# Performance work log

Hardware: AMD Instinct MI355X
Metric: run time of the kernel (lower is better)

Reference implementation:

```python
import jax, jax.numpy as jnp
import numpy as np

NUM_NODES = 100000
NUM_EDGES = 1600000
DIM = 64
TAU = 0.5
EPS = 1e-12
SURGERY_EPS = 1e-6


def setup_inputs() -> dict:
    key = jax.random.key(0)
    k1, k2, k3, k4, k5 = jax.random.split(key, 5)
    x = jax.random.normal(k1, (NUM_NODES, DIM), dtype=jnp.float32)
    edge_index = jax.random.randint(k2, (2, NUM_EDGES), 0, NUM_NODES, dtype=jnp.int64)
    edge_weight = jax.random.uniform(k3, (NUM_EDGES,), dtype=jnp.float32)
    # nn.Linear weights (no bias): y = x @ W.T
    W_self = jax.random.normal(k4, (DIM, DIM), dtype=jnp.float32) / np.sqrt(DIM)
    W_neigh = jax.random.normal(k5, (DIM, DIM), dtype=jnp.float32) / np.sqrt(DIM)
    return {"x": x, "edge_index": edge_index, "edge_weight": edge_weight,
            "W_self": W_self, "W_neigh": W_neigh}


def reference(x, edge_index, edge_weight, W_self, W_neigh):
    num_nodes = x.shape[0]
    row, col = edge_index[0], edge_index[1]

    # --- Ollivier-Ricci (LLY limit-free combinatorial lower-bound) curvature per edge ---
    deg = jax.ops.segment_sum(edge_weight, row, num_segments=num_nodes)  # weighted out-degree
    inv_du = 1.0 / jnp.maximum(deg[row], EPS)
    inv_dv = 1.0 / jnp.maximum(deg[col], EPS)
    kappa = 2.0 * inv_du + 2.0 * inv_dv - 2.0  # [E]

    # --- CFL-stable step size for the Ricci flow ---
    delta_t = 0.5 / (jnp.max(jnp.abs(kappa)) + 1e-6)

    # --- Ricci-flow half step: dw/dt = -kappa * w ---
    w_half = jnp.maximum(edge_weight * (1.0 - 0.5 * delta_t * kappa), 0.0)

    # --- metric surgery: drop degenerate edges (implemented as a zero-weight mask,
    #     keeping edge count static so the kernel is jit-compatible) ---
    mask = w_half > SURGERY_EPS
    w_half = jnp.where(mask, w_half, 0.0)

    # --- row normalisation ---
    row_sum = jax.ops.segment_sum(w_half, row, num_segments=num_nodes)
    w_norm = w_half / jnp.maximum(row_sum[row], EPS)

    # --- Laplacian off-diagonals: L_uv = -w_norm  =>  -L_uv = w_norm ---
    minus_L = w_norm

    # --- incident mean curvature per node (over surviving edges) -> curvature gate ---
    cnt = jax.ops.segment_sum(mask.astype(x.dtype), row, num_segments=num_nodes)
    k_sum = jax.ops.segment_sum(jnp.where(mask, kappa, 0.0), row, num_segments=num_nodes)
    mean_kappa = k_sum / jnp.maximum(cnt, 1.0)
    rho = jax.nn.sigmoid(mean_kappa)  # [N]

    # --- gated message passing ---
    h_self = x @ W_self.T    # [N, D]
    h_neigh = x @ W_neigh.T  # [N, D]
    msg = minus_L[:, None] * h_neigh[col]                      # [E, D] gather + scale
    neigh_aggr = jax.ops.segment_sum(msg, row, num_segments=num_nodes)  # scatter-add

    # h0 buffer == first-forward x (detached)
    out = rho[:, None] * h_self + neigh_aggr + TAU * x
    return out, edge_index, w_norm
```

## Files before the change

kernel.cpp:

```cpp
#include <hip/hip_runtime.h>
#include <math.h>

#define NNODES 100000
#define NEDGES 1600000
#define DIM 64
#define TAU 0.5f
#define EPSF 1e-12f
#define SEPS 1e-6f

#define K 256
#define RPB 391
#define TILE 4096
#define EPT 16
#define CAP 7168
#define MAXK_GRID 512

typedef unsigned long long ull;
typedef unsigned short u16;
typedef __attribute__((ext_vector_type(8))) short bf16x8;
typedef __attribute__((ext_vector_type(4))) float f32x4;

__device__ __forceinline__ float bf2f(u16 h) {
    return __uint_as_float((unsigned)h << 16);
}
__device__ __forceinline__ u16 f2bf(float f) {
    unsigned u = __float_as_uint(f);
    u += 0x7FFFu + ((u >> 16) & 1);
    return (u16)(u >> 16);
}

__global__ __launch_bounds__(256) void k_init(int* __restrict__ bcur) {
    bcur[threadIdx.x] = threadIdx.x * CAP;
}

__global__ __launch_bounds__(256) void k_bin(const int* __restrict__ ei, const float* __restrict__ w,
                                             int* __restrict__ bcur, ull* __restrict__ arena,
                                             int E, int N) {
    __shared__ ull stg[TILE];
    __shared__ unsigned char bkt[TILE];
    __shared__ int cnt[K], lscan[K], gbase[K], cur[K], sc[K];
    __shared__ int tot;
    int t = threadIdx.x;
    int e0 = blockIdx.x * TILE;
    cnt[t] = 0; cur[t] = 0;
    __syncthreads();
    ull rec[EPT];
    int bb[EPT];
#pragma unroll
    for (int j = 0; j < EPT; j++) {
        int e = e0 + t + j * 256;
        bb[j] = -1;
        if (e < E) {
            int r = min(max(ei[e], 0), N - 1);
            int c = min(max(ei[E + e], 0), N - 1);
            float wv = w[e];
            int b = r / RPB, lr = r - b * RPB;
            rec[j] = ((ull)__float_as_uint(wv) << 32) | (unsigned)(c | (lr << 17));
            bb[j] = b;
            atomicAdd(&cnt[b], 1);
        }
    }
    __syncthreads();
    int v = cnt[t];
    sc[t] = v;
    __syncthreads();
    for (int o = 1; o < K; o <<= 1) {
        int a = (t >= o) ? sc[t - o] : 0;
        __syncthreads();
        sc[t] += a;
        __syncthreads();
    }
    lscan[t] = sc[t] - v;
    if (v > 0) gbase[t] = atomicAdd(&bcur[t], v);
    if (t == K - 1) tot = sc[t];
    __syncthreads();
#pragma unroll
    for (int j = 0; j < EPT; j++) {
        if (bb[j] >= 0) {
            int p = lscan[bb[j]] + atomicAdd(&cur[bb[j]], 1);
            stg[p] = rec[j];
            bkt[p] = (unsigned char)bb[j];
        }
    }
    __syncthreads();
    int T = tot;
    for (int i = t; i < T; i += 256) {
        int b = bkt[i];
        size_t pos = (size_t)gbase[b] + (i - lscan[b]);
        if (pos < (size_t)(b + 1) * CAP) arena[pos] = stg[i];
    }
}

__global__ __launch_bounds__(256) void k_sort(const int* __restrict__ bcur,
                                              ull* __restrict__ arena,
                                              float* __restrict__ invdeg,
                                              int* __restrict__ off, int* __restrict__ degi,
                                              int N) {
    __shared__ ull stg[CAP];
    __shared__ int hist[RPB];
    __shared__ float degl[RPB];
    __shared__ int cur[RPB];
    __shared__ int sc[512];
    int t = threadIdx.x, b = blockIdx.x;
    int base = b * CAP;
    int cnt = min(bcur[b] - base, CAP);
    for (int i = t; i < RPB; i += 256) { hist[i] = 0; degl[i] = 0.0f; cur[i] = 0; }
    __syncthreads();
    for (int i = t; i < cnt; i += 256) {
        ull rec = arena[base + i];
        stg[i] = rec;
        int lr = (int)((rec >> 17) & 0x1FF);
        atomicAdd(&hist[lr], 1);
        atomicAdd(&degl[lr], __uint_as_float((unsigned)(rec >> 32)));
    }
    __syncthreads();
    int v0 = (t < RPB) ? hist[t] : 0;
    int v1 = (t + 256 < RPB) ? hist[t + 256] : 0;
    sc[t] = v0; sc[t + 256] = v1;
    __syncthreads();
    for (int o = 1; o < 512; o <<= 1) {
        int a = (t >= o) ? sc[t - o] : 0;
        int c2 = (t + 256 >= o) ? sc[t + 256 - o] : 0;
        __syncthreads();
        sc[t] += a; sc[t + 256] += c2;
        __syncthreads();
    }
    int ex0 = sc[t] - v0, ex1 = sc[t + 256] - v1;
    hist[t] = ex0;
    if (t + 256 < RPB) hist[t + 256] = ex1;
    int rn0 = b * RPB + t;
    if (rn0 < N) {
        off[rn0] = base + ex0; degi[rn0] = v0;
        invdeg[rn0] = 1.0f / fmaxf(degl[t], EPSF);
    }
    int rn1 = rn0 + 256;
    if (t + 256 < RPB && rn1 < N) {
        off[rn1] = base + ex1; degi[rn1] = v1;
        invdeg[rn1] = 1.0f / fmaxf(degl[t + 256], EPSF);
    }
    __syncthreads();
    int2* out2 = (int2*)arena;
    for (int i = t; i < cnt; i += 256) {
        ull rec = stg[i];
        int lr = (int)((rec >> 17) & 0x1FF);
        int p = hist[lr] + atomicAdd(&cur[lr], 1);
        out2[base + p] = make_int2((int)(rec & 0x1FFFF), (int)(unsigned)(rec >> 32));
    }
}

__global__ __launch_bounds__(256) void k_maxk(const int* __restrict__ ei,
                                              const float* __restrict__ invdeg,
                                              float* __restrict__ maxabs, int E, int N) {
    float m = 0.0f;
    int stride = gridDim.x * 256;
    for (int e = blockIdx.x * 256 + threadIdx.x; e < E; e += stride) {
        int r = min(max(ei[e], 0), N - 1);
        int c = min(max(ei[E + e], 0), N - 1);
        m = fmaxf(m, fabsf(2.0f * invdeg[r] + 2.0f * invdeg[c] - 2.0f));
    }
    for (int o = 32; o > 0; o >>= 1) m = fmaxf(m, __shfl_down(m, o, 64));
    __shared__ float red[4];
    int lane = threadIdx.x & 63, wid = threadIdx.x >> 6;
    if (lane == 0) red[wid] = m;
    __syncthreads();
    if (threadIdx.x == 0) {
        float bm = fmaxf(fmaxf(red[0], red[1]), fmaxf(red[2], red[3]));
        atomicMax((unsigned int*)maxabs, __float_as_uint(bm));
    }
}

__global__ void k_node(const int* __restrict__ off, const int* __restrict__ degi,
                       const float* __restrict__ invdeg,
                       const int2* __restrict__ csr, const float* __restrict__ maxabs,
                       float* __restrict__ rho, float* __restrict__ row_sum, int N) {
    int n = blockIdx.x * blockDim.x + threadIdx.x;
    if (n >= N) return;
    int s = off[n], e2 = s + degi[n];
    float dt = 0.5f / (*maxabs + 1e-6f);
    float a = 2.0f * invdeg[n] - 2.0f;
    float rs = 0.0f, ct = 0.0f, ks = 0.0f;
    for (int i = s; i < e2; i++) {
        int2 pr = csr[i];
        float we = __int_as_float(pr.y);
        float kap = a + 2.0f * invdeg[pr.x];
        float wh = fmaxf(we * (1.0f - 0.5f * dt * kap), 0.0f);
        if (wh > SEPS) { rs += wh; ct += 1.0f; ks += kap; }
    }
    float mk = ks / fmaxf(ct, 1.0f);
    rho[n] = 1.0f / (1.0f + expf(-mk));
    row_sum[n] = rs;
}

#define WL(mp, d, kk) (((mp) * 64 + (d)) * 72 + (kk))
__global__ __launch_bounds__(256) void k_gemm(const float* __restrict__ x,
                                              const float* __restrict__ Wself,
                                              const float* __restrict__ Wneigh,
                                              const float* __restrict__ rho,
                                              u16* __restrict__ hneigh_h,
                                              float* __restrict__ out, int N) {
    __shared__ u16 wlds[4 * 64 * 72];
    int t = threadIdx.x;
    for (int i = t; i < 4096; i += 256) {
        int d = i >> 6, k = i & 63;
        float v = Wself[i];
        u16 h = f2bf(v);
        u16 lo = f2bf(v - bf2f(h));
        wlds[WL(0, d, k)] = h;
        wlds[WL(1, d, k)] = lo;
        v = Wneigh[i];
        h = f2bf(v);
        lo = f2bf(v - bf2f(h));
        wlds[WL(2, d, k)] = h;
        wlds[WL(3, d, k)] = lo;
    }
    __syncthreads();
    int w = t >> 6, l = t & 63;
    int m = l & 15, kg = l >> 4;
    int n0 = blockIdx.x * 64 + w * 16;
    if (n0 >= N) return;
    int nodeA = n0 + m;
    bf16x8 ah[2], al[2];
#pragma unroll
    for (int ks = 0; ks < 2; ks++) {
        float v[8];
        if (nodeA < N) {
            const float4* xp = (const float4*)(x + (size_t)nodeA * 64 + ks * 32 + kg * 8);
            float4 v0 = xp[0], v1 = xp[1];
            v[0] = v0.x; v[1] = v0.y; v[2] = v0.z; v[3] = v0.w;
            v[4] = v1.x; v[5] = v1.y; v[6] = v1.z; v[7] = v1.w;
        } else {
#pragma unroll
            for (int j = 0; j < 8; j++) v[j] = 0.0f;
        }
#pragma unroll
        for (int j = 0; j < 8; j++) {
            u16 h = f2bf(v[j]);
            u16 lo = f2bf(v[j] - bf2f(h));
            ah[ks][j] = (short)h;
            al[ks][j] = (short)lo;
        }
    }
    f32x4 accS[4], accN[4];
#pragma unroll
    for (int dt = 0; dt < 4; dt++) {
        accS[dt] = (f32x4){0.0f, 0.0f, 0.0f, 0.0f};
        accN[dt] = (f32x4){0.0f, 0.0f, 0.0f, 0.0f};
    }
#pragma unroll
    for (int dt = 0; dt < 4; dt++) {
        int d = dt * 16 + m;
#pragma unroll
        for (int ks = 0; ks < 2; ks++) {
            int kof = ks * 32 + kg * 8;
            bf16x8 bsh = *(const bf16x8*)&wlds[WL(0, d, kof)];
            bf16x8 bsl = *(const bf16x8*)&wlds[WL(1, d, kof)];
            bf16x8 bnh = *(const bf16x8*)&wlds[WL(2, d, kof)];
            bf16x8 bnl = *(const bf16x8*)&wlds[WL(3, d, kof)];
            accS[dt] = __builtin_amdgcn_mfma_f32_16x16x32_bf16(ah[ks], bsh, accS[dt], 0, 0, 0);
            accS[dt] = __builtin_amdgcn_mfma_f32_16x16x32_bf16(al[ks], bsh, accS[dt], 0, 0, 0);
            accS[dt] = __builtin_amdgcn_mfma_f32_16x16x32_bf16(ah[ks], bsl, accS[dt], 0, 0, 0);
            accN[dt] = __builtin_amdgcn_mfma_f32_16x16x32_bf16(ah[ks], bnh, accN[dt], 0, 0, 0);
            accN[dt] = __builtin_amdgcn_mfma_f32_16x16x32_bf16(al[ks], bnh, accN[dt], 0, 0, 0);
            accN[dt] = __builtin_amdgcn_mfma_f32_16x16x32_bf16(ah[ks], bnl, accN[dt], 0, 0, 0);
        }
    }
    int rbase = kg * 4;
#pragma unroll
    for (int r = 0; r < 4; r++) {
        int nn = n0 + rbase + r;
        if (nn >= N) continue;
        float rh = rho[nn];
#pragma unroll
        for (int dt = 0; dt < 4; dt++) {
            int d = dt * 16 + m;
            size_t idx = (size_t)nn * 64 + d;
            out[idx] = rh * accS[dt][r] + TAU * x[idx];
            hneigh_h[idx] = f2bf(accN[dt][r]);
        }
    }
}

__global__ __launch_bounds__(256) void k_aggr(const int* __restrict__ off,
                                              const int* __restrict__ degi,
                                              const float* __restrict__ invdeg,
                                              const int2* __restrict__ csr,
                                              const float* __restrict__ row_sum,
                                              const float* __restrict__ maxabs,
                                              const u16* __restrict__ hneigh_h,
                                              float* __restrict__ out, int N) {
    int t = threadIdx.x;
    int lane = t & 63;
    int q = lane & 15;
    int g = lane >> 4;
    int n = blockIdx.x * 4 + (t >> 6);
    if (n >= N) return;
    int s = off[n], end = s + degi[n];
    float dt = 0.5f / (*maxabs + 1e-6f);
    float c1 = -0.5f * dt;
    float a = 2.0f * invdeg[n] - 2.0f;
    float inv_rs = 1.0f / fmaxf(row_sum[n], EPSF);
    const ushort4* hn4 = (const ushort4*)hneigh_h;
    float a0 = 0.0f, a1 = 0.0f, a2 = 0.0f, a3 = 0.0f;
    int i = s;
    for (; i + 16 <= end; i += 16) {
        int2 p0 = csr[i + g];
        int2 p1 = csr[i + 4 + g];
        int2 p2 = csr[i + 8 + g];
        int2 p3 = csr[i + 12 + g];
        ushort4 h0 = hn4[(unsigned)((p0.x << 4) | q)];
        ushort4 h1 = hn4[(unsigned)((p1.x << 4) | q)];
        ushort4 h2 = hn4[(unsigned)((p2.x << 4) | q)];
        ushort4 h3 = hn4[(unsigned)((p3.x << 4) | q)];
        float k0 = fmaf(2.0f, invdeg[p0.x], a), k1 = fmaf(2.0f, invdeg[p1.x], a);
        float k2 = fmaf(2.0f, invdeg[p2.x], a), k3 = fmaf(2.0f, invdeg[p3.x], a);
        float w0 = __int_as_float(p0.y) * fmaf(c1, k0, 1.0f);
        float w1 = __int_as_float(p1.y) * fmaf(c1, k1, 1.0f);
        float w2 = __int_as_float(p2.y) * fmaf(c1, k2, 1.0f);
        float w3 = __int_as_float(p3.y) * fmaf(c1, k3, 1.0f);
        w0 = (w0 > SEPS) ? w0 : 0.0f;
        w1 = (w1 > SEPS) ? w1 : 0.0f;
        w2 = (w2 > SEPS) ? w2 : 0.0f;
        w3 = (w3 > SEPS) ? w3 : 0.0f;
        a0 = fmaf(w0, bf2f(h0.x), a0); a1 = fmaf(w0, bf2f(h0.y), a1);
        a2 = fmaf(w0, bf2f(h0.z), a2); a3 = fmaf(w0, bf2f(h0.w), a3);
        a0 = fmaf(w1, bf2f(h1.x), a0); a1 = fmaf(w1, bf2f(h1.y), a1);
        a2 = fmaf(w1, bf2f(h1.z), a2); a3 = fmaf(w1, bf2f(h1.w), a3);
        a0 = fmaf(w2, bf2f(h2.x), a0); a1 = fmaf(w2, bf2f(h2.y), a1);
        a2 = fmaf(w2, bf2f(h2.z), a2); a3 = fmaf(w2, bf2f(h2.w), a3);
        a0 = fmaf(w3, bf2f(h3.x), a0); a1 = fmaf(w3, bf2f(h3.y), a1);
        a2 = fmaf(w3, bf2f(h3.z), a2); a3 = fmaf(w3, bf2f(h3.w), a3);
    }
    for (; i + 8 <= end; i += 8) {
        int2 p0 = csr[i + g];
        int2 p1 = csr[i + 4 + g];
        ushort4 h0 = hn4[(unsigned)((p0.x << 4) | q)];
        ushort4 h1 = hn4[(unsigned)((p1.x << 4) | q)];
        float k0 = fmaf(2.0f, invdeg[p0.x], a), k1 = fmaf(2.0f, invdeg[p1.x], a);
        float w0 = __int_as_float(p0.y) * fmaf(c1, k0, 1.0f);
        float w1 = __int_as_float(p1.y) * fmaf(c1, k1, 1.0f);
        w0 = (w0 > SEPS) ? w0 : 0.0f;
        w1 = (w1 > SEPS) ? w1 : 0.0f;
        a0 = fmaf(w0, bf2f(h0.x), a0); a1 = fmaf(w0, bf2f(h0.y), a1);
        a2 = fmaf(w0, bf2f(h0.z), a2); a3 = fmaf(w0, bf2f(h0.w), a3);
        a0 = fmaf(w1, bf2f(h1.x), a0); a1 = fmaf(w1, bf2f(h1.y), a1);
        a2 = fmaf(w1, bf2f(h1.z), a2); a3 = fmaf(w1, bf2f(h1.w), a3);
    }
    for (; i < end; i += 4) {
        int e = i + g;
        bool v = e < end;
        int2 p = make_int2(0, 0);
        if (v) p = csr[e];
        ushort4 h = hn4[(unsigned)((p.x << 4) | q)];
        float kk = fmaf(2.0f, invdeg[p.x], a);
        float wv = __int_as_float(p.y) * fmaf(c1, kk, 1.0f);
        wv = (v && wv > SEPS) ? wv : 0.0f;
        a0 = fmaf(wv, bf2f(h.x), a0);
        a1 = fmaf(wv, bf2f(h.y), a1);
        a2 = fmaf(wv, bf2f(h.z), a2);
        a3 = fmaf(wv, bf2f(h.w), a3);
    }
    a0 += __shfl_xor(a0, 16, 64);
    a1 += __shfl_xor(a1, 16, 64);
    a2 += __shfl_xor(a2, 16, 64);
    a3 += __shfl_xor(a3, 16, 64);
    a0 += __shfl_xor(a0, 32, 64);
    a1 += __shfl_xor(a1, 32, 64);
    a2 += __shfl_xor(a2, 32, 64);
    a3 += __shfl_xor(a3, 32, 64);
    if (g == 0) {
        float4* o4 = (float4*)(out + (size_t)n * 64);
        float4 o = o4[q];
        o.x += a0 * inv_rs;
        o.y += a1 * inv_rs;
        o.z += a2 * inv_rs;
        o.w += a3 * inv_rs;
        o4[q] = o;
    }
}

__global__ void k_final(const int* __restrict__ ei, const float* __restrict__ w,
                        const float* __restrict__ invdeg, const float* __restrict__ row_sum,
                        const float* __restrict__ maxabs,
                        float* __restrict__ out_ei, float* __restrict__ out_wn, int E, int N) {
    int e = blockIdx.x * blockDim.x + threadIdx.x;
    if (e >= E) return;
    int r0 = ei[e], c0 = ei[E + e];
    int r = min(max(r0, 0), N - 1);
    int c = min(max(c0, 0), N - 1);
    float dt = 0.5f / (*maxabs + 1e-6f);
    float kap = 2.0f * invdeg[r] + 2.0f * invdeg[c] - 2.0f;
    float wh = fmaxf(w[e] * (1.0f - 0.5f * dt * kap), 0.0f);
    if (wh <= SEPS) wh = 0.0f;
    out_wn[e] = wh / fmaxf(row_sum[r], EPSF);
    out_ei[e] = (float)r0;
    out_ei[E + e] = (float)c0;
}

extern "C" void kernel_launch(void* const* d_in, const int* in_sizes, int n_in,
                              void* d_out, int out_size, void* d_ws, size_t ws_size,
                              hipStream_t stream) {
    (void)in_sizes; (void)n_in; (void)out_size; (void)ws_size;
    const int N = NNODES, E = NEDGES;

    const float* x      = (const float*)d_in[0];
    const int*   ei     = (const int*)d_in[1];
    const float* w      = (const float*)d_in[2];
    const float* Wself  = (const float*)d_in[3];
    const float* Wneigh = (const float*)d_in[4];

    float* out    = (float*)d_out;
    float* out_ei = out + (size_t)N * DIM;
    float* out_wn = out_ei + 2 * (size_t)E;

    ull*  arena = (ull*)out_ei;
    int2* csr   = (int2*)out_ei;

    float* invdeg  = (float*)d_ws;
    int*   off     = (int*)d_ws + (size_t)N;
    int*   degi    = (int*)d_ws + 2 * (size_t)N;
    float* rho     = (float*)d_ws + 3 * (size_t)N;
    float* row_sum = rho + (size_t)N;
    float* maxabs  = row_sum + (size_t)N;
    int*   bcur    = (int*)(maxabs + 4);
    u16*   hneigh_h = (u16*)((float*)d_ws + 5 * (size_t)N + 288);

    hipMemsetAsync((void*)maxabs, 0, 4 * sizeof(float), stream);

    k_init<<<1, 256, 0, stream>>>(bcur);
    k_bin<<<(E + TILE - 1) / TILE, 256, 0, stream>>>(ei, w, bcur, arena, E, N);
    k_sort<<<K, 256, 0, stream>>>(bcur, arena, invdeg, off, degi, N);
    k_maxk<<<MAXK_GRID, 256, 0, stream>>>(ei, invdeg, maxabs, E, N);
    k_node<<<(N + 255) / 256, 256, 0, stream>>>(off, degi, invdeg, csr, maxabs, rho, row_sum, N);
    k_gemm<<<(N + 63) / 64, 256, 0, stream>>>(x, Wself, Wneigh, rho, hneigh_h, out, N);
    k_aggr<<<(N + 3) / 4, 256, 0, stream>>>(off, degi, invdeg, csr, row_sum, maxabs,
                                            hneigh_h, out, N);
    k_final<<<(E + 255) / 256, 256, 0, stream>>>(ei, w, invdeg, row_sum, maxabs,
                                                 out_ei, out_wn, E, N);
}
```

Baseline: 261.8 us.

## Precompute half-step weights into CSR and replace per-node loop with bin-parallel kernel

The per-node curvature/row-sum kernel, which had one thread walk each node's edges serially, is replaced by a bin-level kernel. It processes each sorted bucket's edges in parallel, using shared-memory atomics per local row. That kernel also writes the surgery-masked half-step weight back into the CSR record and keeps the local row index in the upper bits of the column field. The aggregation kernel then reads the precomputed weight directly and no longer gathers invdeg per edge or recomputes kappa. The costs are an extra write pass over the CSR array and a mask on every column index.

```diff
diff --git a/kernel.cpp b/kernel.cpp
--- a/kernel.cpp
+++ b/kernel.cpp
@@ -144,7 +144,7 @@
         ull rec = stg[i];
         int lr = (int)((rec >> 17) & 0x1FF);
         int p = hist[lr] + atomicAdd(&cur[lr], 1);
-        out2[base + p] = make_int2((int)(rec & 0x1FFFF), (int)(unsigned)(rec >> 32));
+        out2[base + p] = make_int2((int)(rec & 0x3FFFFFF), (int)(unsigned)(rec >> 32));
     }
 }
 
@@ -169,26 +169,49 @@
     }
 }
 
-__global__ void k_node(const int* __restrict__ off, const int* __restrict__ degi,
-                       const float* __restrict__ invdeg,
-                       const int2* __restrict__ csr, const float* __restrict__ maxabs,
-                       float* __restrict__ rho, float* __restrict__ row_sum, int N) {
-    int n = blockIdx.x * blockDim.x + threadIdx.x;
-    if (n >= N) return;
-    int s = off[n], e2 = s + degi[n];
+__global__ __launch_bounds__(256) void k_wh(const int* __restrict__ bcur,
+                                            const float* __restrict__ invdeg,
+                                            int2* __restrict__ csr,
+                                            const float* __restrict__ maxabs,
+                                            float* __restrict__ rho,
+                                            float* __restrict__ row_sum, int N) {
+    __shared__ float ivl[RPB], rs[RPB], ks[RPB];
+    __shared__ int ct[RPB];
+    int t = threadIdx.x, b = blockIdx.x;
+    int base = b * CAP;
+    int cnt = min(bcur[b] - base, CAP);
+    int r0 = b * RPB;
+    for (int i = t; i < RPB; i += 256) {
+        int rn = r0 + i;
+        ivl[i] = (rn < N) ? invdeg[rn] : 0.0f;
+        rs[i] = 0.0f; ks[i] = 0.0f; ct[i] = 0;
+    }
+    __syncthreads();
     float dt = 0.5f / (*maxabs + 1e-6f);
-    float a = 2.0f * invdeg[n] - 2.0f;
-    float rs = 0.0f, ct = 0.0f, ks = 0.0f;
-    for (int i = s; i < e2; i++) {
-        int2 pr = csr[i];
-        float we = __int_as_float(pr.y);
-        float kap = a + 2.0f * invdeg[pr.x];
-        float wh = fmaxf(we * (1.0f - 0.5f * dt * kap), 0.0f);
-        if (wh > SEPS) { rs += wh; ct += 1.0f; ks += kap; }
-    }
-    float mk = ks / fmaxf(ct, 1.0f);
-    rho[n] = 1.0f / (1.0f + expf(-mk));
-    row_sum[n] = rs;
+    for (int i = t; i < cnt; i += 256) {
+        int2 rec = csr[base + i];
+        int col = rec.x & 0x1FFFF;
+        int lr = rec.x >> 17;
+        float kap = 2.0f * (ivl[lr] + invdeg[col]) - 2.0f;
+        float wh = fmaxf(__int_as_float(rec.y) * (1.0f - 0.5f * dt * kap), 0.0f);
+        if (wh > SEPS) {
+            atomicAdd(&rs[lr], wh);
+            atomicAdd(&ks[lr], kap);
+            atomicAdd(&ct[lr], 1);
+        } else {
+            wh = 0.0f;
+        }
+        csr[base + i] = make_int2(rec.x, __float_as_int(wh));
+    }
+    __syncthreads();
+    for (int i = t; i < RPB; i += 256) {
+        int rn = r0 + i;
+        if (rn < N) {
+            float mk = ks[i] / fmaxf((float)ct[i], 1.0f);
+            rho[rn] = 1.0f / (1.0f + expf(-mk));
+            row_sum[rn] = rs[i];
+        }
+    }
 }
 
 #define WL(mp, d, kk) (((mp) * 64 + (d)) * 72 + (kk))
@@ -282,10 +305,8 @@
 
 __global__ __launch_bounds__(256) void k_aggr(const int* __restrict__ off,
                                               const int* __restrict__ degi,
-                                              const float* __restrict__ invdeg,
                                               const int2* __restrict__ csr,
                                               const float* __restrict__ row_sum,
-                                              const float* __restrict__ maxabs,
                                               const u16* __restrict__ hneigh_h,
                                               float* __restrict__ out, int N) {
     int t = threadIdx.x;
@@ -295,9 +316,6 @@
     int n = blockIdx.x * 4 + (t >> 6);
     if (n >= N) return;
     int s = off[n], end = s + degi[n];
-    float dt = 0.5f / (*maxabs + 1e-6f);
-    float c1 = -0.5f * dt;
-    float a = 2.0f * invdeg[n] - 2.0f;
     float inv_rs = 1.0f / fmaxf(row_sum[n], EPSF);
     const ushort4* hn4 = (const ushort4*)hneigh_h;
     float a0 = 0.0f, a1 = 0.0f, a2 = 0.0f, a3 = 0.0f;
@@ -307,20 +325,12 @@
         int2 p1 = csr[i + 4 + g];
         int2 p2 = csr[i + 8 + g];
         int2 p3 = csr[i + 12 + g];
-        ushort4 h0 = hn4[(unsigned)((p0.x << 4) | q)];
-        ushort4 h1 = hn4[(unsigned)((p1.x << 4) | q)];
-        ushort4 h2 = hn4[(unsigned)((p2.x << 4) | q)];
-        ushort4 h3 = hn4[(unsigned)((p3.x << 4) | q)];
-        float k0 = fmaf(2.0f, invdeg[p0.x], a), k1 = fmaf(2.0f, invdeg[p1.x], a);
-        float k2 = fmaf(2.0f, invdeg[p2.x], a), k3 = fmaf(2.0f, invdeg[p3.x], a);
-        float w0 = __int_as_float(p0.y) * fmaf(c1, k0, 1.0f);
-        float w1 = __int_as_float(p1.y) * fmaf(c1, k1, 1.0f);
-        float w2 = __int_as_float(p2.y) * fmaf(c1, k2, 1.0f);
-        float w3 = __int_as_float(p3.y) * fmaf(c1, k3, 1.0f);
-        w0 = (w0 > SEPS) ? w0 : 0.0f;
-        w1 = (w1 > SEPS) ? w1 : 0.0f;
-        w2 = (w2 > SEPS) ? w2 : 0.0f;
-        w3 = (w3 > SEPS) ? w3 : 0.0f;
+        ushort4 h0 = hn4[(unsigned)(((p0.x & 0x1FFFF) << 4) | q)];
+        ushort4 h1 = hn4[(unsigned)(((p1.x & 0x1FFFF) << 4) | q)];
+        ushort4 h2 = hn4[(unsigned)(((p2.x & 0x1FFFF) << 4) | q)];
+        ushort4 h3 = hn4[(unsigned)(((p3.x & 0x1FFFF) << 4) | q)];
+        float w0 = __int_as_float(p0.y), w1 = __int_as_float(p1.y);
+        float w2 = __int_as_float(p2.y), w3 = __int_as_float(p3.y);
         a0 = fmaf(w0, bf2f(h0.x), a0); a1 = fmaf(w0, bf2f(h0.y), a1);
         a2 = fmaf(w0, bf2f(h0.z), a2); a3 = fmaf(w0, bf2f(h0.w), a3);
         a0 = fmaf(w1, bf2f(h1.x), a0); a1 = fmaf(w1, bf2f(h1.y), a1);
@@ -333,13 +343,9 @@
     for (; i + 8 <= end; i += 8) {
         int2 p0 = csr[i + g];
         int2 p1 = csr[i + 4 + g];
-        ushort4 h0 = hn4[(unsigned)((p0.x << 4) | q)];
-        ushort4 h1 = hn4[(unsigned)((p1.x << 4) | q)];
-        float k0 = fmaf(2.0f, invdeg[p0.x], a), k1 = fmaf(2.0f, invdeg[p1.x], a);
-        float w0 = __int_as_float(p0.y) * fmaf(c1, k0, 1.0f);
-        float w1 = __int_as_float(p1.y) * fmaf(c1, k1, 1.0f);
-        w0 = (w0 > SEPS) ? w0 : 0.0f;
-        w1 = (w1 > SEPS) ? w1 : 0.0f;
+        ushort4 h0 = hn4[(unsigned)(((p0.x & 0x1FFFF) << 4) | q)];
+        ushort4 h1 = hn4[(unsigned)(((p1.x & 0x1FFFF) << 4) | q)];
+        float w0 = __int_as_float(p0.y), w1 = __int_as_float(p1.y);
         a0 = fmaf(w0, bf2f(h0.x), a0); a1 = fmaf(w0, bf2f(h0.y), a1);
         a2 = fmaf(w0, bf2f(h0.z), a2); a3 = fmaf(w0, bf2f(h0.w), a3);
         a0 = fmaf(w1, bf2f(h1.x), a0); a1 = fmaf(w1, bf2f(h1.y), a1);
@@ -350,10 +356,8 @@
         bool v = e < end;
         int2 p = make_int2(0, 0);
         if (v) p = csr[e];
-        ushort4 h = hn4[(unsigned)((p.x << 4) | q)];
-        float kk = fmaf(2.0f, invdeg[p.x], a);
-        float wv = __int_as_float(p.y) * fmaf(c1, kk, 1.0f);
-        wv = (v && wv > SEPS) ? wv : 0.0f;
+        ushort4 h = hn4[(unsigned)(((p.x & 0x1FFFF) << 4) | q)];
+        float wv = v ? __int_as_float(p.y) : 0.0f;
         a0 = fmaf(wv, bf2f(h.x), a0);
         a1 = fmaf(wv, bf2f(h.y), a1);
         a2 = fmaf(wv, bf2f(h.z), a2);
@@ -430,10 +434,9 @@
     k_bin<<<(E + TILE - 1) / TILE, 256, 0, stream>>>(ei, w, bcur, arena, E, N);
     k_sort<<<K, 256, 0, stream>>>(bcur, arena, invdeg, off, degi, N);
     k_maxk<<<MAXK_GRID, 256, 0, stream>>>(ei, invdeg, maxabs, E, N);
-    k_node<<<(N + 255) / 256, 256, 0, stream>>>(off, degi, invdeg, csr, maxabs, rho, row_sum, N);
+    k_wh<<<K, 256, 0, stream>>>(bcur, invdeg, csr, maxabs, rho, row_sum, N);
     k_gemm<<<(N + 63) / 64, 256, 0, stream>>>(x, Wself, Wneigh, rho, hneigh_h, out, N);
-    k_aggr<<<(N + 3) / 4, 256, 0, stream>>>(off, degi, invdeg, csr, row_sum, maxabs,
-                                            hneigh_h, out, N);
+    k_aggr<<<(N + 3) / 4, 256, 0, stream>>>(off, degi, csr, row_sum, hneigh_h, out, N);
     k_final<<<(E + 255) / 256, 256, 0, stream>>>(ei, w, invdeg, row_sum, maxabs,
                                                  out_ei, out_wn, E, N);
 }
```

New measurement: 269.3 us. +2.9%, slower.

## Fuse per-node curvature stats into aggregation kernel and drop k_node

Applied to the files above, without the earlier changes.

Removes the separate k_node pass over the CSR. k_aggr now accumulates row_sum, the curvature sum and the surviving-edge count during its neighbour loop. It then computes rho and applies the rho*h_self + tau*x epilogue, and k_gemm writes raw h_self. The memset is folded into k_init, and the 8-edge remainder loop is dropped. This removes one kernel launch and a full CSR and invdeg re-read, at the cost of a few extra reductions per aggregation and an x read moved into k_aggr.

```diff
diff --git a/kernel.cpp b/kernel.cpp
--- a/kernel.cpp
+++ b/kernel.cpp
@@ -29,8 +29,10 @@
     return (u16)(u >> 16);
 }
 
-__global__ __launch_bounds__(256) void k_init(int* __restrict__ bcur) {
+__global__ __launch_bounds__(256) void k_init(int* __restrict__ bcur,
+                                              float* __restrict__ maxabs) {
     bcur[threadIdx.x] = threadIdx.x * CAP;
+    if (threadIdx.x < 4) maxabs[threadIdx.x] = 0.0f;
 }
 
 __global__ __launch_bounds__(256) void k_bin(const int* __restrict__ ei, const float* __restrict__ w,
@@ -169,33 +171,10 @@
     }
 }
 
-__global__ void k_node(const int* __restrict__ off, const int* __restrict__ degi,
-                       const float* __restrict__ invdeg,
-                       const int2* __restrict__ csr, const float* __restrict__ maxabs,
-                       float* __restrict__ rho, float* __restrict__ row_sum, int N) {
-    int n = blockIdx.x * blockDim.x + threadIdx.x;
-    if (n >= N) return;
-    int s = off[n], e2 = s + degi[n];
-    float dt = 0.5f / (*maxabs + 1e-6f);
-    float a = 2.0f * invdeg[n] - 2.0f;
-    float rs = 0.0f, ct = 0.0f, ks = 0.0f;
-    for (int i = s; i < e2; i++) {
-        int2 pr = csr[i];
-        float we = __int_as_float(pr.y);
-        float kap = a + 2.0f * invdeg[pr.x];
-        float wh = fmaxf(we * (1.0f - 0.5f * dt * kap), 0.0f);
-        if (wh > SEPS) { rs += wh; ct += 1.0f; ks += kap; }
-    }
-    float mk = ks / fmaxf(ct, 1.0f);
-    rho[n] = 1.0f / (1.0f + expf(-mk));
-    row_sum[n] = rs;
-}
-
 #define WL(mp, d, kk) (((mp) * 64 + (d)) * 72 + (kk))
 __global__ __launch_bounds__(256) void k_gemm(const float* __restrict__ x,
                                               const float* __restrict__ Wself,
                                               const float* __restrict__ Wneigh,
-                                              const float* __restrict__ rho,
                                               u16* __restrict__ hneigh_h,
                                               float* __restrict__ out, int N) {
     __shared__ u16 wlds[4 * 64 * 72];
@@ -269,12 +248,11 @@
     for (int r = 0; r < 4; r++) {
         int nn = n0 + rbase + r;
         if (nn >= N) continue;
-        float rh = rho[nn];
 #pragma unroll
         for (int dt = 0; dt < 4; dt++) {
             int d = dt * 16 + m;
             size_t idx = (size_t)nn * 64 + d;
-            out[idx] = rh * accS[dt][r] + TAU * x[idx];
+            out[idx] = accS[dt][r];
             hneigh_h[idx] = f2bf(accN[dt][r]);
         }
     }
@@ -284,9 +262,10 @@
                                               const int* __restrict__ degi,
                                               const float* __restrict__ invdeg,
                                               const int2* __restrict__ csr,
-                                              const float* __restrict__ row_sum,
                                               const float* __restrict__ maxabs,
+                                              const float* __restrict__ x,
                                               const u16* __restrict__ hneigh_h,
+                                              float* __restrict__ row_sum,
                                               float* __restrict__ out, int N) {
     int t = threadIdx.x;
     int lane = t & 63;
@@ -298,9 +277,9 @@
     float dt = 0.5f / (*maxabs + 1e-6f);
     float c1 = -0.5f * dt;
     float a = 2.0f * invdeg[n] - 2.0f;
-    float inv_rs = 1.0f / fmaxf(row_sum[n], EPSF);
     const ushort4* hn4 = (const ushort4*)hneigh_h;
     float a0 = 0.0f, a1 = 0.0f, a2 = 0.0f, a3 = 0.0f;
+    float rs = 0.0f, ks = 0.0f, ct = 0.0f;
     int i = s;
     for (; i + 16 <= end; i += 16) {
         int2 p0 = csr[i + g];
@@ -317,10 +296,14 @@
         float w1 = __int_as_float(p1.y) * fmaf(c1, k1, 1.0f);
         float w2 = __int_as_float(p2.y) * fmaf(c1, k2, 1.0f);
         float w3 = __int_as_float(p3.y) * fmaf(c1, k3, 1.0f);
-        w0 = (w0 > SEPS) ? w0 : 0.0f;
-        w1 = (w1 > SEPS) ? w1 : 0.0f;
-        w2 = (w2 > SEPS) ? w2 : 0.0f;
-        w3 = (w3 > SEPS) ? w3 : 0.0f;
+        bool m0 = w0 > SEPS, m1 = w1 > SEPS, m2 = w2 > SEPS, m3 = w3 > SEPS;
+        w0 = m0 ? w0 : 0.0f;
+        w1 = m1 ? w1 : 0.0f;
+        w2 = m2 ? w2 : 0.0f;
+        w3 = m3 ? w3 : 0.0f;
+        rs += (w0 + w1) + (w2 + w3);
+        ks += ((m0 ? k0 : 0.0f) + (m1 ? k1 : 0.0f)) + ((m2 ? k2 : 0.0f) + (m3 ? k3 : 0.0f));
+        ct += ((m0 ? 1.0f : 0.0f) + (m1 ? 1.0f : 0.0f)) + ((m2 ? 1.0f : 0.0f) + (m3 ? 1.0f : 0.0f));
         a0 = fmaf(w0, bf2f(h0.x), a0); a1 = fmaf(w0, bf2f(h0.y), a1);
         a2 = fmaf(w0, bf2f(h0.z), a2); a3 = fmaf(w0, bf2f(h0.w), a3);
         a0 = fmaf(w1, bf2f(h1.x), a0); a1 = fmaf(w1, bf2f(h1.y), a1);
@@ -330,21 +313,6 @@
         a0 = fmaf(w3, bf2f(h3.x), a0); a1 = fmaf(w3, bf2f(h3.y), a1);
         a2 = fmaf(w3, bf2f(h3.z), a2); a3 = fmaf(w3, bf2f(h3.w), a3);
     }
-    for (; i + 8 <= end; i += 8) {
-        int2 p0 = csr[i + g];
-        int2 p1 = csr[i + 4 + g];
-        ushort4 h0 = hn4[(unsigned)((p0.x << 4) | q)];
-        ushort4 h1 = hn4[(unsigned)((p1.x << 4) | q)];
-        float k0 = fmaf(2.0f, invdeg[p0.x], a), k1 = fmaf(2.0f, invdeg[p1.x], a);
-        float w0 = __int_as_float(p0.y) * fmaf(c1, k0, 1.0f);
-        float w1 = __int_as_float(p1.y) * fmaf(c1, k1, 1.0f);
-        w0 = (w0 > SEPS) ? w0 : 0.0f;
-        w1 = (w1 > SEPS) ? w1 : 0.0f;
-        a0 = fmaf(w0, bf2f(h0.x), a0); a1 = fmaf(w0, bf2f(h0.y), a1);
-        a2 = fmaf(w0, bf2f(h0.z), a2); a3 = fmaf(w0, bf2f(h0.w), a3);
-        a0 = fmaf(w1, bf2f(h1.x), a0); a1 = fmaf(w1, bf2f(h1.y), a1);
-        a2 = fmaf(w1, bf2f(h1.z), a2); a3 = fmaf(w1, bf2f(h1.w), a3);
-    }
     for (; i < end; i += 4) {
         int e = i + g;
         bool v = e < end;
@@ -353,7 +321,11 @@
         ushort4 h = hn4[(unsigned)((p.x << 4) | q)];
         float kk = fmaf(2.0f, invdeg[p.x], a);
         float wv = __int_as_float(p.y) * fmaf(c1, kk, 1.0f);
-        wv = (v && wv > SEPS) ? wv : 0.0f;
+        bool m = v && (wv > SEPS);
+        wv = m ? wv : 0.0f;
+        rs += wv;
+        ks += m ? kk : 0.0f;
+        ct += m ? 1.0f : 0.0f;
         a0 = fmaf(wv, bf2f(h.x), a0);
         a1 = fmaf(wv, bf2f(h.y), a1);
         a2 = fmaf(wv, bf2f(h.z), a2);
@@ -363,18 +335,30 @@
     a1 += __shfl_xor(a1, 16, 64);
     a2 += __shfl_xor(a2, 16, 64);
     a3 += __shfl_xor(a3, 16, 64);
+    rs += __shfl_xor(rs, 16, 64);
+    ks += __shfl_xor(ks, 16, 64);
+    ct += __shfl_xor(ct, 16, 64);
     a0 += __shfl_xor(a0, 32, 64);
     a1 += __shfl_xor(a1, 32, 64);
     a2 += __shfl_xor(a2, 32, 64);
     a3 += __shfl_xor(a3, 32, 64);
+    rs += __shfl_xor(rs, 32, 64);
+    ks += __shfl_xor(ks, 32, 64);
+    ct += __shfl_xor(ct, 32, 64);
+    float mk = ks / fmaxf(ct, 1.0f);
+    float rho = 1.0f / (1.0f + expf(-mk));
+    float inv_rs = 1.0f / fmaxf(rs, EPSF);
     if (g == 0) {
         float4* o4 = (float4*)(out + (size_t)n * 64);
+        const float4* x4 = (const float4*)(x + (size_t)n * 64);
         float4 o = o4[q];
-        o.x += a0 * inv_rs;
-        o.y += a1 * inv_rs;
-        o.z += a2 * inv_rs;
-        o.w += a3 * inv_rs;
+        float4 xv = x4[q];
+        o.x = fmaf(rho, o.x, fmaf(TAU, xv.x, a0 * inv_rs));
+        o.y = fmaf(rho, o.y, fmaf(TAU, xv.y, a1 * inv_rs));
+        o.z = fmaf(rho, o.z, fmaf(TAU, xv.z, a2 * inv_rs));
+        o.w = fmaf(rho, o.w, fmaf(TAU, xv.w, a3 * inv_rs));
         o4[q] = o;
+        if (q == 0) row_sum[n] = rs;
     }
 }
 
@@ -418,22 +402,18 @@
     float* invdeg  = (float*)d_ws;
     int*   off     = (int*)d_ws + (size_t)N;
     int*   degi    = (int*)d_ws + 2 * (size_t)N;
-    float* rho     = (float*)d_ws + 3 * (size_t)N;
-    float* row_sum = rho + (size_t)N;
+    float* row_sum = (float*)d_ws + 3 * (size_t)N;
     float* maxabs  = row_sum + (size_t)N;
     int*   bcur    = (int*)(maxabs + 4);
-    u16*   hneigh_h = (u16*)((float*)d_ws + 5 * (size_t)N + 288);
-
-    hipMemsetAsync((void*)maxabs, 0, 4 * sizeof(float), stream);
-
-    k_init<<<1, 256, 0, stream>>>(bcur);
+    u16*   hneigh_h = (u16*)((float*)d_ws + 4 * (size_t)N + 288);
+
+    k_init<<<1, 256, 0, stream>>>(bcur, maxabs);
     k_bin<<<(E + TILE - 1) / TILE, 256, 0, stream>>>(ei, w, bcur, arena, E, N);
     k_sort<<<K, 256, 0, stream>>>(bcur, arena, invdeg, off, degi, N);
     k_maxk<<<MAXK_GRID, 256, 0, stream>>>(ei, invdeg, maxabs, E, N);
-    k_node<<<(N + 255) / 256, 256, 0, stream>>>(off, degi, invdeg, csr, maxabs, rho, row_sum, N);
-    k_gemm<<<(N + 63) / 64, 256, 0, stream>>>(x, Wself, Wneigh, rho, hneigh_h, out, N);
-    k_aggr<<<(N + 3) / 4, 256, 0, stream>>>(off, degi, invdeg, csr, row_sum, maxabs,
-                                            hneigh_h, out, N);
+    k_gemm<<<(N + 63) / 64, 256, 0, stream>>>(x, Wself, Wneigh, hneigh_h, out, N);
+    k_aggr<<<(N + 3) / 4, 256, 0, stream>>>(off, degi, invdeg, csr, maxabs, x,
+                                            hneigh_h, row_sum, out, N);
     k_final<<<(E + 255) / 256, 256, 0, stream>>>(ei, w, invdeg, row_sum, maxabs,
                                                  out_ei, out_wn, E, N);
 }
```

Result: faster. 249.4 us (-4.7%).
